# Kernel tuning notes

Measured on AMD Instinct MI355X. Metric: run time of the kernel, lower is better.

## Reference

```python
import jax, jax.numpy as jnp
import numpy as np

B, T, C, H, N = 4, 1024, 2048, 32, 64
DFF, DW, DV, DA, DG = 8192, 64, 32, 64, 128
GN_EPS = 64e-5  # RWKV7 ln_x GroupNorm eps


def _ln(x, w, b, eps=1e-5):
    m = x.mean(-1, keepdims=True)
    v = ((x - m) ** 2).mean(-1, keepdims=True)
    return (x - m) / jnp.sqrt(v + eps) * w + b


def _block(x, v_first, att_shift, ffn_shift, wkv_state,
           ln1_w, ln1_b, ln2_w, ln2_b,
           x_r, x_w, x_k, x_v, x_a, x_g,
           Wr, Wk, Wv, Wo,
           w0, w1, w2, v0, v1, v2, a0, a1, a2, g1, g2,
           k_k, k_a, r_k, lnx_w, lnx_b,
           ffn_xk, Wk_ffn, Wv_ffn):
    # ----- TimeMix -----
    xn = _ln(x, ln1_w, ln1_b)
    xx = jnp.concatenate([att_shift[:, None, :], xn[:, :-1]], axis=1) - xn
    xr = xn + xx * x_r
    xw = xn + xx * x_w
    xk_ = xn + xx * x_k
    xv = xn + xx * x_v
    xa = xn + xx * x_a
    xg = xn + xx * x_g

    r = xr @ Wr
    w = -jax.nn.softplus(-(w0 + jnp.tanh(xw @ w1) @ w2)) - 0.5  # <= -0.5
    k = xk_ @ Wk
    v = xv @ Wv
    # layer_id != 0: interpolate toward v_first
    v = v + (v_first - v) * jax.nn.sigmoid(v0 + (xv @ v1) @ v2)
    a = jax.nn.sigmoid(a0 + (xa @ a1) @ a2)
    g = jax.nn.sigmoid(xg @ g1) @ g2

    kk = (k * k_k).reshape(B, T, H, N)
    kk = kk / jnp.maximum(jnp.linalg.norm(kk, axis=-1, keepdims=True), 1e-12)
    k = k * (1.0 + (a - 1.0) * k_a)

    rh = r.reshape(B, T, H, N)
    wh = jnp.exp(-jnp.exp(w.reshape(B, T, H, N)))  # decay in (0,1)
    kh = k.reshape(B, T, H, N)
    vh = v.reshape(B, T, H, N)
    ah = a.reshape(B, T, H, N)
    aa = -kk
    bb = kk * ah

    def step(S, inp):
        # S: [B,H,N(value),N(key)]
        r_t, w_t, k_t, v_t, a_t, b_t = inp
        sa = jnp.einsum('bhvk,bhk->bhv', S, a_t)
        S = S * w_t[:, :, None, :] + sa[..., None] * b_t[:, :, None, :] + v_t[..., None] * k_t[:, :, None, :]
        y = jnp.einsum('bhvk,bhk->bhv', S, r_t)
        return S, y

    tm = lambda z: jnp.swapaxes(z, 0, 1)  # [B,T,H,N] -> [T,B,H,N]
    S_new, ys = jax.lax.scan(step, wkv_state, (tm(rh), tm(wh), tm(kh), tm(vh), tm(aa), tm(bb)))
    x_wkv = jnp.swapaxes(ys, 0, 1).reshape(B, T, C)

    # GroupNorm over H groups of size N (RWKV7 ln_x)
    xh = x_wkv.reshape(B, T, H, N)
    mu = xh.mean(-1, keepdims=True)
    var = ((xh - mu) ** 2).mean(-1, keepdims=True)
    x_wkv = ((xh - mu) / jnp.sqrt(var + GN_EPS)).reshape(B, T, C) * lnx_w + lnx_b

    resid = ((rh * kh * r_k).sum(-1, keepdims=True) * vh).reshape(B, T, C)
    x_wkv = x_wkv + resid
    att_out = (x_wkv * g) @ Wo
    x1 = x + att_out

    # ----- ChannelMix -----
    xn2 = _ln(x1, ln2_w, ln2_b)
    xx2 = jnp.concatenate([ffn_shift[:, None, :], xn2[:, :-1]], axis=1) - xn2
    xkf = xn2 + xx2 * ffn_xk
    kf = jnp.square(jax.nn.relu(xkf @ Wk_ffn))
    x_out = x1 + kf @ Wv_ffn
    return x_out, S_new


def setup_inputs() -> dict:
    ks = jax.random.split(jax.random.key(0), 48)
    rn = lambda i, sh, s=1.0: jax.random.normal(ks[i], sh, dtype=jnp.float32) * s
    return {
        'x': rn(0, (B, T, C)), 'v_first': rn(1, (B, T, C)),
        'att_shift': rn(2, (B, C)), 'ffn_shift': rn(3, (B, C)),
        'wkv_state': jnp.zeros((B, H, N, N), jnp.float32),
        'ln1_w': jnp.ones((C,), jnp.float32), 'ln1_b': jnp.zeros((C,), jnp.float32),
        'ln2_w': jnp.ones((C,), jnp.float32), 'ln2_b': jnp.zeros((C,), jnp.float32),
        'x_r': rn(4, (C,), 0.3), 'x_w': rn(5, (C,), 0.3), 'x_k': rn(6, (C,), 0.3),
        'x_v': rn(7, (C,), 0.3), 'x_a': rn(8, (C,), 0.3), 'x_g': rn(9, (C,), 0.3),
        'Wr': rn(10, (C, C), 0.02), 'Wk': rn(11, (C, C), 0.02),
        'Wv': rn(12, (C, C), 0.02), 'Wo': rn(13, (C, C), 0.02),
        'w0': rn(14, (C,), 0.3), 'w1': rn(15, (C, DW), 0.02), 'w2': rn(16, (DW, C), 0.02),
        'v0': rn(17, (C,), 0.3), 'v1': rn(18, (C, DV), 0.02), 'v2': rn(19, (DV, C), 0.02),
        'a0': rn(20, (C,), 0.3), 'a1': rn(21, (C, DA), 0.02), 'a2': rn(22, (DA, C), 0.02),
        'g1': rn(23, (C, DG), 0.02), 'g2': rn(24, (DG, C), 0.02),
        'k_k': rn(25, (C,), 0.1) + 0.7, 'k_a': rn(26, (C,), 0.1) + 0.7, 'r_k': rn(27, (H, N), 0.1),
        'lnx_w': jnp.ones((C,), jnp.float32), 'lnx_b': jnp.zeros((C,), jnp.float32),
        'ffn_xk': rn(28, (C,), 0.3), 'Wk_ffn': rn(29, (C, DFF), 0.02), 'Wv_ffn': rn(30, (DFF, C), 0.02),
    }


def reference(x, v_first, att_shift, ffn_shift, wkv_state,
              ln1_w, ln1_b, ln2_w, ln2_b,
              x_r, x_w, x_k, x_v, x_a, x_g,
              Wr, Wk, Wv, Wo,
              w0, w1, w2, v0, v1, v2, a0, a1, a2, g1, g2,
              k_k, k_a, r_k, lnx_w, lnx_b,
              ffn_xk, Wk_ffn, Wv_ffn):
    return _block(x, v_first, att_shift, ffn_shift, wkv_state,
                  ln1_w, ln1_b, ln2_w, ln2_b,
                  x_r, x_w, x_k, x_v, x_a, x_g,
                  Wr, Wk, Wv, Wo,
                  w0, w1, w2, v0, v1, v2, a0, a1, a2, g1, g2,
                  k_k, k_a, r_k, lnx_w, lnx_b,
                  ffn_xk, Wk_ffn, Wv_ffn)
```

## Files before the change

kernel.cpp:

```cpp
#include <hip/hip_runtime.h>
#include <cstdint>


typedef __attribute__((ext_vector_type(4))) float f32x4;
typedef __attribute__((ext_vector_type(8))) __bf16 bf16x8;
typedef __attribute__((ext_vector_type(8))) unsigned short us8;

#define DEV __device__ __forceinline__

DEV unsigned short f2b(float f) {
  union { float f; unsigned u; } v; v.f = f;
  unsigned r = v.u + 0x7fffu + ((v.u >> 16) & 1u);
  return (unsigned short)(r >> 16);
}
DEV float b2f(unsigned short u) {
  union { unsigned u; float f; } v; v.u = (unsigned)u << 16;
  return v.f;
}

DEV void gload16(const void* g, void* l) {
  void* gg = const_cast<void*>(g);
  __builtin_amdgcn_global_load_lds(
      (__attribute__((address_space(1))) unsigned int*)gg,
      (__attribute__((address_space(3))) unsigned int*)l, 16, 0, 0);
}

DEV float red8(float v) {
  v += __shfl_xor(v, 1);
  v += __shfl_xor(v, 2);
  v += __shfl_xor(v, 4);
  return v;
}


__global__ void k_transpose(const float* __restrict__ src,
                            unsigned short* __restrict__ dst, int R, int Cc) {
  __shared__ float tile[32][33];
  const int c0 = blockIdx.x * 32, r0 = blockIdx.y * 32;
  const int tx = threadIdx.x, ty = threadIdx.y;
  for (int i = ty; i < 32; i += 8)
    tile[i][tx] = src[(size_t)(r0 + i) * Cc + c0 + tx];
  __syncthreads();
  for (int i = ty; i < 32; i += 8)
    dst[(size_t)(c0 + i) * R + r0 + tx] = f2b(tile[tx][i]);
}

__global__ void k_wcat(const float* __restrict__ w1, const float* __restrict__ a1,
                       const float* __restrict__ v1, const float* __restrict__ g1,
                       const float* __restrict__ xw, const float* __restrict__ xa,
                       const float* __restrict__ xv, const float* __restrict__ xg,
                       unsigned short* __restrict__ dst) {
  const int i = blockIdx.x * 256 + threadIdx.x;
  if (i >= 384 * 4096) return;
  const int j = i >> 12, c = i & 4095;
  float val = 0.f;
  if (j < 288) {
    const float* W; const float* mix; int jj, D;
    if (j < 64)       { W = w1; mix = xw; jj = j;       D = 64;  }
    else if (j < 128) { W = a1; mix = xa; jj = j - 64;  D = 64;  }
    else if (j < 160) { W = v1; mix = xv; jj = j - 128; D = 32;  }
    else              { W = g1; mix = xg; jj = j - 160; D = 128; }
    const int cc = c & 2047;
    val = W[(size_t)cc * D + jj];
    if (c >= 2048) val *= mix[cc];
  }
  dst[i] = f2b(val);
}


DEV void breduce2(float& a, float& b, float* rbuf) {
#pragma unroll
  for (int m = 1; m < 64; m <<= 1) { a += __shfl_xor(a, m); b += __shfl_xor(b, m); }
  const int wid = threadIdx.x >> 6, lane = threadIdx.x & 63;
  if (lane == 0) { rbuf[wid] = a; rbuf[4 + wid] = b; }
  __syncthreads();
  a = rbuf[0] + rbuf[1] + rbuf[2] + rbuf[3];
  b = rbuf[4] + rbuf[5] + rbuf[6] + rbuf[7];
  __syncthreads();
}

__global__ __launch_bounds__(256)
void k_ln1_mix(const float* __restrict__ x, const float* __restrict__ shift,
               const float* __restrict__ lw, const float* __restrict__ lb,
               const float* __restrict__ mr, const float* __restrict__ mk,
               const float* __restrict__ mv,
               unsigned short* __restrict__ A2, unsigned short* __restrict__ xrb,
               unsigned short* __restrict__ xkb, unsigned short* __restrict__ xvb) {
  __shared__ float rbuf[8];
  const int m = blockIdx.x, tid = threadIdx.x;
  const int b = m >> 10, t = m & 1023;
  const float* xt = x + (size_t)m * 2048 + tid * 8;
  const float* xp = (t > 0) ? (x + (size_t)(m - 1) * 2048 + tid * 8)
                            : (shift + (size_t)b * 2048 + tid * 8);
  float vt[8], vp[8];
  *(float4*)&vt[0] = *(const float4*)(xt);
  *(float4*)&vt[4] = *(const float4*)(xt + 4);
  *(float4*)&vp[0] = *(const float4*)(xp);
  *(float4*)&vp[4] = *(const float4*)(xp + 4);
  float st = 0.f, sp = 0.f;
#pragma unroll
  for (int i = 0; i < 8; ++i) { st += vt[i]; sp += vp[i]; }
  breduce2(st, sp, rbuf);
  const float mt_ = st * (1.f / 2048.f), mp_ = sp * (1.f / 2048.f);
  float qt = 0.f, qp = 0.f;
#pragma unroll
  for (int i = 0; i < 8; ++i) {
    float d0 = vt[i] - mt_; qt += d0 * d0;
    float d1 = vp[i] - mp_; qp += d1 * d1;
  }
  breduce2(qt, qp, rbuf);
  const float rt = rsqrtf(qt * (1.f / 2048.f) + 1e-5f);
  const float rp = rsqrtf(qp * (1.f / 2048.f) + 1e-5f);
  const bool lnp = (t > 0);
#pragma unroll
  for (int i = 0; i < 8; ++i) {
    const int c = tid * 8 + i;
    const float wv = lw[c], bv = lb[c];
    const float xn = (vt[i] - mt_) * rt * wv + bv;
    const float pn = lnp ? ((vp[i] - mp_) * rp * wv + bv) : vp[i];
    const float xx = pn - xn;
    A2[(size_t)m * 4096 + c] = f2b(xn);
    A2[(size_t)m * 4096 + 2048 + c] = f2b(xx);
    xrb[(size_t)m * 2048 + c] = f2b(xn + xx * mr[c]);
    xkb[(size_t)m * 2048 + c] = f2b(xn + xx * mk[c]);
    xvb[(size_t)m * 2048 + c] = f2b(xn + xx * mv[c]);
  }
}

__global__ __launch_bounds__(256)
void k_ln2_mix(const float* __restrict__ x1, const float* __restrict__ shift,
               const float* __restrict__ lw, const float* __restrict__ lb,
               const float* __restrict__ mk, unsigned short* __restrict__ xkf) {
  __shared__ float rbuf[8];
  const int m = blockIdx.x, tid = threadIdx.x;
  const int b = m >> 10, t = m & 1023;
  const float* xt = x1 + (size_t)m * 2048 + tid * 8;
  const float* xp = (t > 0) ? (x1 + (size_t)(m - 1) * 2048 + tid * 8)
                            : (shift + (size_t)b * 2048 + tid * 8);
  float vt[8], vp[8];
  *(float4*)&vt[0] = *(const float4*)(xt);
  *(float4*)&vt[4] = *(const float4*)(xt + 4);
  *(float4*)&vp[0] = *(const float4*)(xp);
  *(float4*)&vp[4] = *(const float4*)(xp + 4);
  float st = 0.f, sp = 0.f;
#pragma unroll
  for (int i = 0; i < 8; ++i) { st += vt[i]; sp += vp[i]; }
  breduce2(st, sp, rbuf);
  const float mt_ = st * (1.f / 2048.f), mp_ = sp * (1.f / 2048.f);
  float qt = 0.f, qp = 0.f;
#pragma unroll
  for (int i = 0; i < 8; ++i) {
    float d0 = vt[i] - mt_; qt += d0 * d0;
    float d1 = vp[i] - mp_; qp += d1 * d1;
  }
  breduce2(qt, qp, rbuf);
  const float rt = rsqrtf(qt * (1.f / 2048.f) + 1e-5f);
  const float rp = rsqrtf(qp * (1.f / 2048.f) + 1e-5f);
  const bool lnp = (t > 0);
#pragma unroll
  for (int i = 0; i < 8; ++i) {
    const int c = tid * 8 + i;
    const float wv = lw[c], bv = lb[c];
    const float xn = (vt[i] - mt_) * rt * wv + bv;
    const float pn = lnp ? ((vp[i] - mp_) * rp * wv + bv) : vp[i];
    xkf[(size_t)m * 2048 + c] = f2b(xn + (pn - xn) * mk[c]);
  }
}


constexpr int EP_F32 = 0, EP_B16 = 1, EP_W = 2, EP_AB16 = 3, EP_VGB16 = 4,
              EP_RELU2 = 5, EP_ADDF = 6, EP_HACT = 7;

template <int EP>
DEV void ep_store(float acc, long row, long c, long ldc, float* Co,
                  unsigned short* Cob, const float* bias, const float* e0f,
                  const unsigned short* e0b) {
  const long idx = row * ldc + c;
  if constexpr (EP == EP_F32) {
    Co[idx] = acc;
  } else if constexpr (EP == EP_B16) {
    Cob[idx] = f2b(acc);
  } else if constexpr (EP == EP_W) {
    const float wv = bias[c] + acc;
    const float sp = log1pf(expf(-wv));
    const float w = -sp - 0.5f;
    Co[idx] = expf(-expf(w));
  } else if constexpr (EP == EP_AB16) {
    Cob[idx] = f2b(1.f / (1.f + expf(-(bias[c] + acc))));
  } else if constexpr (EP == EP_VGB16) {
    const float s = 1.f / (1.f + expf(-(bias[c] + acc)));
    const float vv = b2f(e0b[idx]);
    Cob[idx] = f2b(vv + (e0f[idx] - vv) * s);
  } else if constexpr (EP == EP_RELU2) {
    const float r = fmaxf(acc, 0.f);
    Cob[idx] = f2b(r * r);
  } else if constexpr (EP == EP_ADDF) {
    Co[idx] = acc + e0f[idx];
  } else if constexpr (EP == EP_HACT) {
    float vv = acc;
    if (c < 64) vv = tanhf(vv);
    else if (c >= 160) vv = 1.f / (1.f + expf(-vv));
    Cob[idx] = f2b(vv);
  }
}


template <int EP>
__global__ __launch_bounds__(256)
void gemm_bt(const unsigned short* __restrict__ A, long lda,
             const unsigned short* __restrict__ Bt, long ldb, long N, long K,
             long ldc, float* __restrict__ Co, unsigned short* __restrict__ Cob,
             const float* __restrict__ bias, const float* __restrict__ e0f,
             const unsigned short* __restrict__ e0b) {
  __shared__ unsigned short As[4096];
  __shared__ unsigned short Bs[4096];
  const int tid = threadIdx.x;
  const int wid = tid >> 6, lane = tid & 63;
  const long row0 = (long)blockIdx.x * 128, col0 = (long)blockIdx.y * 128;
  const int wm = (wid >> 1) * 64, wn = (wid & 1) * 64;
  f32x4 acc[4][4] = {};
  const int sr = tid >> 2, sk = (tid & 3) * 8;
  const unsigned short* gA = A + (row0 + sr) * lda + sk;
  const unsigned short* gB = Bt + (col0 + sr) * ldb + sk;
  unsigned short* lA = As + wid * 512;
  unsigned short* lB = Bs + wid * 512;
  const int fr = lane & 15, fk = (lane >> 4) * 8;

  for (long kb = 0; kb < K; kb += 32) {
    gload16(gA + kb, lA);
    gload16(gA + kb + 64 * lda, lA + 2048);
    gload16(gB + kb, lB);
    gload16(gB + kb + 64 * ldb, lB + 2048);
    __syncthreads();
    bf16x8 af[4], bq[4];
#pragma unroll
    for (int mt = 0; mt < 4; ++mt)
      af[mt] = *(const bf16x8*)(As + (wm + mt * 16 + fr) * 32 + fk);
#pragma unroll
    for (int nt = 0; nt < 4; ++nt)
      bq[nt] = *(const bf16x8*)(Bs + (wn + nt * 16 + fr) * 32 + fk);
#pragma unroll
    for (int mt = 0; mt < 4; ++mt)
#pragma unroll
      for (int nt = 0; nt < 4; ++nt)
        acc[mt][nt] = __builtin_amdgcn_mfma_f32_16x16x32_bf16(
            af[mt], bq[nt], acc[mt][nt], 0, 0, 0);
    __syncthreads();
  }
  const int fq = lane >> 4;
#pragma unroll
  for (int mt = 0; mt < 4; ++mt) {
#pragma unroll
    for (int nt = 0; nt < 4; ++nt) {
      const long c = col0 + wn + nt * 16 + fr;
      if (c < N) {
        const long rb = row0 + wm + mt * 16 + fq * 4;
#pragma unroll
        for (int rg = 0; rg < 4; ++rg)
          ep_store<EP>(acc[mt][nt][rg], rb + rg, c, ldc, Co, Cob, bias, e0f, e0b);
      }
    }
  }
}


template <int EP>
__global__ __launch_bounds__(512)
void gemm2(const unsigned short* __restrict__ A, long lda,
           const unsigned short* __restrict__ Bt, long ldb, long K, long ldc,
           float* __restrict__ Co, unsigned short* __restrict__ Cob,
           const float* __restrict__ e0f) {
  __shared__ unsigned short As[2][4096];
  __shared__ unsigned short Bs[2][8192];
  const int tid = threadIdx.x;
  const int wid = tid >> 6, lane = tid & 63;
  const long row0 = (long)blockIdx.x * 128, col0 = (long)blockIdx.y * 256;
  const int wm = (wid >> 2) * 64, wn = (wid & 3) * 64;
  f32x4 acc[4][4] = {};
  const int srow = tid >> 2;
  const int scol = 8 * ((tid & 3) ^ (srow & 3));
  const unsigned short* gA = A + (row0 + srow) * lda + scol;
  const unsigned short* gB1 = Bt + (col0 + srow) * ldb + scol;
  const unsigned short* gB2 = gB1 + 128 * ldb;
  const int fr = lane & 15, fc = lane >> 4;

#define STAGE2(buf, kb)                                   \
  {                                                       \
    gload16(gA + (kb), &As[buf][0] + wid * 512);          \
    gload16(gB1 + (kb), &Bs[buf][0] + wid * 512);         \
    gload16(gB2 + (kb), &Bs[buf][0] + 4096 + wid * 512);  \
  }

  STAGE2(0, 0)
  const int NT = (int)(K >> 5);
  int cur = 0;
  for (int kt = 0; kt < NT; ++kt) {
    if (kt + 1 < NT) {
      STAGE2(cur ^ 1, (long)(kt + 1) * 32)
      asm volatile("s_waitcnt vmcnt(3)" ::: "memory");
    } else {
      asm volatile("s_waitcnt vmcnt(0)" ::: "memory");
    }
    __builtin_amdgcn_s_barrier();
    asm volatile("" ::: "memory");
    bf16x8 af[4], bq[4];
#pragma unroll
    for (int mt = 0; mt < 4; ++mt) {
      const int r = wm + mt * 16 + fr;
      af[mt] = *(const bf16x8*)(&As[cur][0] + r * 32 + ((fc ^ (r & 3)) * 8));
    }
#pragma unroll
    for (int nt = 0; nt < 4; ++nt) {
      const int r = wn + nt * 16 + fr;
      bq[nt] = *(const bf16x8*)(&Bs[cur][0] + r * 32 + ((fc ^ (r & 3)) * 8));
    }
    __builtin_amdgcn_s_setprio(1);
#pragma unroll
    for (int mt = 0; mt < 4; ++mt)
#pragma unroll
      for (int nt = 0; nt < 4; ++nt)
        acc[mt][nt] = __builtin_amdgcn_mfma_f32_16x16x32_bf16(
            af[mt], bq[nt], acc[mt][nt], 0, 0, 0);
    __builtin_amdgcn_s_setprio(0);
    asm volatile("" ::: "memory");
    __builtin_amdgcn_s_barrier();
    cur ^= 1;
  }
#undef STAGE2
  const int fq = lane >> 4;
#pragma unroll
  for (int mt = 0; mt < 4; ++mt) {
#pragma unroll
    for (int nt = 0; nt < 4; ++nt) {
      const long c = col0 + wn + nt * 16 + fr;
      const long rb = row0 + wm + mt * 16 + fq * 4;
#pragma unroll
      for (int rg = 0; rg < 4; ++rg)
        ep_store<EP>(acc[mt][nt][rg], rb + rg, c, ldc, Co, Cob, nullptr, e0f,
                     nullptr);
    }
  }
}

__global__ __launch_bounds__(256)
void k_post(unsigned short* __restrict__ kio, unsigned short* __restrict__ abio,
            unsigned short* __restrict__ aao, const float* __restrict__ kkw,
            const float* __restrict__ kaw) {
  const int m = blockIdx.x, tid = threadIdx.x;
  const size_t base = (size_t)m * 2048 + tid * 8;
  us8 k8 = *(const us8*)(kio + base);
  us8 a8 = *(const us8*)(abio + base);
  float kk8[8], ka8[8];
  *(float4*)&kk8[0] = *(const float4*)(kkw + tid * 8);
  *(float4*)&kk8[4] = *(const float4*)(kkw + tid * 8 + 4);
  *(float4*)&ka8[0] = *(const float4*)(kaw + tid * 8);
  *(float4*)&ka8[4] = *(const float4*)(kaw + tid * 8 + 4);
  float kx[8], kv[8], av[8];
  float ss = 0.f;
#pragma unroll
  for (int i = 0; i < 8; ++i) {
    kv[i] = b2f(k8[i]); av[i] = b2f(a8[i]);
    kx[i] = kv[i] * kk8[i]; ss += kx[i] * kx[i];
  }
  ss = red8(ss);
  const float inv = 1.f / fmaxf(sqrtf(ss), 1e-12f);
  us8 kh8, aa8, bb8;
#pragma unroll
  for (int i = 0; i < 8; ++i) {
    const float kkn = kx[i] * inv;
    kh8[i] = f2b(kv[i] * (1.f + (av[i] - 1.f) * ka8[i]));
    aa8[i] = f2b(-kkn);
    bb8[i] = f2b(kkn * av[i]);
  }
  *(us8*)(kio + base) = kh8;
  *(us8*)(aao + base) = aa8;
  *(us8*)(abio + base) = bb8;
}


DEV float red16(float x) {
  union { float f; int i; } a, r;
  a.f = x; r.i = __builtin_amdgcn_update_dpp(0, a.i, 0xB1, 0xf, 0xf, true);
  x += r.f;
  a.f = x; r.i = __builtin_amdgcn_update_dpp(0, a.i, 0x4E, 0xf, 0xf, true);
  x += r.f;
  a.f = x; r.i = __builtin_amdgcn_update_dpp(0, a.i, 0x124, 0xf, 0xf, true);
  x += r.f;
  a.f = x; r.i = __builtin_amdgcn_update_dpp(0, a.i, 0x128, 0xf, 0xf, true);
  x += r.f;
  return x;
}

DEV void cv4(const uint2 q, float* o) {
  union { unsigned u; float f; } t;
  t.u = q.x << 16;          o[0] = t.f;
  t.u = q.x & 0xffff0000u;  o[1] = t.f;
  t.u = q.y << 16;          o[2] = t.f;
  t.u = q.y & 0xffff0000u;  o[3] = t.f;
}

__global__ __launch_bounds__(64)
void k_scan(const unsigned short* __restrict__ rp,
            const unsigned short* __restrict__ kp,
            const unsigned short* __restrict__ vp,
            const float* __restrict__ wp,
            const unsigned short* __restrict__ ap,
            const unsigned short* __restrict__ bp,
            const float* __restrict__ s0, unsigned short* __restrict__ yout,
            float* __restrict__ snew) {
  __shared__ float4 slots[8][49];
  __shared__ unsigned short ylds[1024][4];
  const int lane = threadIdx.x;
  const int bh = blockIdx.x & 127;
  const int rq = blockIdx.x >> 7;
  const int b = bh >> 5, h = bh & 31;
  const int kg = lane & 15, rl = lane >> 4;
  const int v = rq * 4 + rl, ks = kg * 4;
  const size_t off_bh = (size_t)b * 1024 * 2048 + (size_t)h * 64;

  float S[4];
  *(float4*)&S[0] = *(const float4*)(s0 + (((size_t)bh * 64 + v) * 64 + ks));

  const char* gp = nullptr;
  size_t gstep = 0;
  if (lane < 49) {
    if (lane < 32) {
      const int arr = lane >> 3, sub = lane & 7;
      const unsigned short* base = arr == 0 ? rp : arr == 1 ? kp
                                 : arr == 2 ? ap : bp;
      gp = (const char*)(base + off_bh + sub * 8);
      gstep = 4096;
    } else if (lane < 48) {
      gp = (const char*)(wp + off_bh + (lane - 32) * 4);
      gstep = 8192;
    } else {
      gp = (const char*)(vp + off_bh + (rq & ~1) * 4);
      gstep = 4096;
    }
  }
#pragma unroll
  for (int s = 0; s < 8; ++s) {
    if (lane < 49) gload16(gp, &slots[s][0]);
    gp += gstep;
  }

  for (int t = 0; t < 1024; ++t) {
    asm volatile("s_waitcnt vmcnt(7)" ::: "memory");
    const int sl = t & 7;
    const char* sb = (const char*)&slots[sl][0];
    uint2 r2 = *(const uint2*)(sb + kg * 8);
    uint2 k2 = *(const uint2*)(sb + 128 + kg * 8);
    uint2 a2 = *(const uint2*)(sb + 256 + kg * 8);
    uint2 b2 = *(const uint2*)(sb + 384 + kg * 8);
    float4 wf = *(const float4*)(sb + 512 + kg * 16);
    const unsigned short vfu =
        *(const unsigned short*)(sb + 768 + ((rq & 1) * 4 + rl) * 2);
    asm volatile("s_waitcnt lgkmcnt(0)" ::: "memory");
    if (lane < 49) gload16(gp, &slots[sl][0]);
    if (t < 1015) gp += gstep;

    float rr[4], kk[4], av[4], bv[4];
    cv4(r2, rr); cv4(k2, kk); cv4(a2, av); cv4(b2, bv);
    const float vv = b2f(vfu);
    float sa = S[0] * av[0] + S[1] * av[1] + S[2] * av[2] + S[3] * av[3];
    sa = red16(sa);
    float y;
    S[0] = S[0] * wf.x + sa * bv[0] + vv * kk[0]; y  = S[0] * rr[0];
    S[1] = S[1] * wf.y + sa * bv[1] + vv * kk[1]; y += S[1] * rr[1];
    S[2] = S[2] * wf.z + sa * bv[2] + vv * kk[2]; y += S[2] * rr[2];
    S[3] = S[3] * wf.w + sa * bv[3] + vv * kk[3]; y += S[3] * rr[3];
    y = red16(y);
    if (kg == 0) ylds[t][rl] = f2b(y);
  }

  *(float4*)(snew + (((size_t)bh * 64 + v) * 64 + ks)) = *(const float4*)&S[0];
  asm volatile("s_waitcnt lgkmcnt(0)" ::: "memory");
#pragma unroll 4
  for (int it = 0; it < 16; ++it) {
    const int t = lane + it * 64;
    const uint2 val = *(const uint2*)&ylds[t][0];
    *(uint2*)(yout + off_bh + (size_t)t * 2048 + rq * 4) = val;
  }
}


__global__ __launch_bounds__(256)
void k_gn(const unsigned short* __restrict__ y, const unsigned short* __restrict__ r,
          const unsigned short* __restrict__ kh, const unsigned short* __restrict__ vf,
          const unsigned short* __restrict__ g, const float* __restrict__ rk,
          const float* __restrict__ lw, const float* __restrict__ lb,
          unsigned short* __restrict__ ywg) {
  const int m = blockIdx.x, tid = threadIdx.x;
  const size_t base = (size_t)m * 2048 + tid * 8;
  us8 y8 = *(const us8*)(y + base);
  us8 r8 = *(const us8*)(r + base);
  us8 k8 = *(const us8*)(kh + base);
  us8 v8 = *(const us8*)(vf + base);
  us8 g8 = *(const us8*)(g + base);
  float yv[8];
  float rkv[8];
  *(float4*)&rkv[0] = *(const float4*)(rk + tid * 8);
  *(float4*)&rkv[4] = *(const float4*)(rk + tid * 8 + 4);
  float sy = 0.f, sd = 0.f;
#pragma unroll
  for (int i = 0; i < 8; ++i) {
    yv[i] = b2f(y8[i]);
    sy += yv[i];
    sd += b2f(r8[i]) * b2f(k8[i]) * rkv[i];
  }
  sy = red8(sy);
  sd = red8(sd);
  const float mu = sy * (1.f / 64.f);
  float sq = 0.f;
#pragma unroll
  for (int i = 0; i < 8; ++i) { const float d = yv[i] - mu; sq += d * d; }
  sq = red8(sq);
  const float rstd = rsqrtf(sq * (1.f / 64.f) + 64e-5f);
  us8 o8;
#pragma unroll
  for (int i = 0; i < 8; ++i) {
    const int c = tid * 8 + i;
    const float gn = (yv[i] - mu) * rstd * lw[c] + lb[c];
    o8[i] = f2b((gn + sd * b2f(v8[i])) * b2f(g8[i]));
  }
  *(us8*)(ywg + base) = o8;
}


extern "C" void kernel_launch(void* const* d_in, const int* in_sizes, int n_in,
                              void* d_out, int out_size, void* d_ws,
                              size_t ws_size, hipStream_t stream) {
  (void)in_sizes; (void)n_in; (void)out_size; (void)ws_size;
  const float* x         = (const float*)d_in[0];
  const float* v_first   = (const float*)d_in[1];
  const float* att_shift = (const float*)d_in[2];
  const float* ffn_shift = (const float*)d_in[3];
  const float* wkv0      = (const float*)d_in[4];
  const float* ln1w = (const float*)d_in[5];
  const float* ln1b = (const float*)d_in[6];
  const float* ln2w = (const float*)d_in[7];
  const float* ln2b = (const float*)d_in[8];
  const float* x_r = (const float*)d_in[9];
  const float* x_w = (const float*)d_in[10];
  const float* x_k = (const float*)d_in[11];
  const float* x_v = (const float*)d_in[12];
  const float* x_a = (const float*)d_in[13];
  const float* x_g = (const float*)d_in[14];
  const float* Wr = (const float*)d_in[15];
  const float* Wk = (const float*)d_in[16];
  const float* Wv = (const float*)d_in[17];
  const float* Wo = (const float*)d_in[18];
  const float* w0 = (const float*)d_in[19];
  const float* w1 = (const float*)d_in[20];
  const float* w2 = (const float*)d_in[21];
  const float* v0 = (const float*)d_in[22];
  const float* v1 = (const float*)d_in[23];
  const float* v2 = (const float*)d_in[24];
  const float* a0 = (const float*)d_in[25];
  const float* a1 = (const float*)d_in[26];
  const float* a2 = (const float*)d_in[27];
  const float* g1 = (const float*)d_in[28];
  const float* g2 = (const float*)d_in[29];
  const float* k_k = (const float*)d_in[30];
  const float* k_a = (const float*)d_in[31];
  const float* r_k = (const float*)d_in[32];
  const float* lnxw = (const float*)d_in[33];
  const float* lnxb = (const float*)d_in[34];
  const float* ffn_xk = (const float*)d_in[35];
  const float* Wkf = (const float*)d_in[36];
  const float* Wvf = (const float*)d_in[37];

  char* ws = (char*)d_ws;
  constexpr size_t OFF_TWR   = 0;
  constexpr size_t OFF_TWK   = 8388608;
  constexpr size_t OFF_TWV   = 16777216;
  constexpr size_t OFF_TWO   = 25165824;
  constexpr size_t OFF_TW2   = 33554432;
  constexpr size_t OFF_TA2   = 33816576;
  constexpr size_t OFF_TV2   = 34078720;
  constexpr size_t OFF_TG2   = 34209792;
  constexpr size_t OFF_TWCAT = 34734080;
  constexpr size_t OFF_HACT  = 37879808;
  constexpr size_t OFF_GBUF  = 40239104;
  constexpr size_t OFF_WH    = 57016320;
  constexpr size_t OFF_R     = 90570752;
  constexpr size_t OFF_KH    = 107347968;
  constexpr size_t OFF_VF    = 124125184;
  constexpr size_t OFF_AA    = 140902400;
  constexpr size_t OFF_BB    = 157679616;

  unsigned short* tWr = (unsigned short*)(ws + OFF_TWR);
  unsigned short* tWk = (unsigned short*)(ws + OFF_TWK);
  unsigned short* tWv = (unsigned short*)(ws + OFF_TWV);
  unsigned short* tWo = (unsigned short*)(ws + OFF_TWO);
  unsigned short* tw2 = (unsigned short*)(ws + OFF_TW2);
  unsigned short* ta2 = (unsigned short*)(ws + OFF_TA2);
  unsigned short* tv2 = (unsigned short*)(ws + OFF_TV2);
  unsigned short* tg2 = (unsigned short*)(ws + OFF_TG2);
  unsigned short* tWcat = (unsigned short*)(ws + OFF_TWCAT);
  unsigned short* Hact  = (unsigned short*)(ws + OFF_HACT);
  unsigned short* gbuf  = (unsigned short*)(ws + OFF_GBUF);
  unsigned short* tWvfh = (unsigned short*)(ws + OFF_GBUF);
  unsigned short* act2  = (unsigned short*)(ws + OFF_WH);
  float*          whb   = (float*)(ws + OFF_WH);
  unsigned short* ywg   = (unsigned short*)(ws + OFF_WH);
  unsigned short* kf    = (unsigned short*)(ws + OFF_WH);
  unsigned short* bxr   = (unsigned short*)(ws + OFF_AA);
  unsigned short* bxk   = (unsigned short*)(ws + OFF_BB);
  unsigned short* bxv   = (unsigned short*)(ws + OFF_VF);
  unsigned short* rbuf  = (unsigned short*)(ws + OFF_R);
  unsigned short* khb   = (unsigned short*)(ws + OFF_KH);
  unsigned short* vfb   = (unsigned short*)(ws + OFF_VF);
  unsigned short* aab   = (unsigned short*)(ws + OFF_AA);
  unsigned short* bbb   = (unsigned short*)(ws + OFF_BB);
  unsigned short* vraw  = (unsigned short*)(ws + OFF_AA);
  unsigned short* abuf  = (unsigned short*)(ws + OFF_BB);
  float*          x1    = (float*)(ws + OFF_R);
  unsigned short* xkf   = (unsigned short*)(ws + OFF_VF);
  unsigned short* tWkf  = (unsigned short*)(ws + OFF_AA);
  float* out = (float*)d_out;
  float* snew = out + 8388608;

  const dim3 tb(32, 8);
  k_transpose<<<dim3(64, 64), tb, 0, stream>>>(Wr, tWr, 2048, 2048);
  k_transpose<<<dim3(64, 64), tb, 0, stream>>>(Wk, tWk, 2048, 2048);
  k_transpose<<<dim3(64, 64), tb, 0, stream>>>(Wv, tWv, 2048, 2048);
  k_transpose<<<dim3(64, 64), tb, 0, stream>>>(Wo, tWo, 2048, 2048);
  k_transpose<<<dim3(64, 2), tb, 0, stream>>>(w2, tw2, 64, 2048);
  k_transpose<<<dim3(64, 2), tb, 0, stream>>>(a2, ta2, 64, 2048);
  k_transpose<<<dim3(64, 1), tb, 0, stream>>>(v2, tv2, 32, 2048);
  k_transpose<<<dim3(64, 4), tb, 0, stream>>>(g2, tg2, 128, 2048);
  k_wcat<<<6144, 256, 0, stream>>>(w1, a1, v1, g1, x_w, x_a, x_v, x_g, tWcat);

  k_ln1_mix<<<4096, 256, 0, stream>>>(x, att_shift, ln1w, ln1b, x_r, x_k, x_v,
                                      act2, bxr, bxk, bxv);
  gemm2<EP_B16><<<dim3(32, 8), 512, 0, stream>>>(
      bxr, 2048, tWr, 2048, 2048, 2048, nullptr, rbuf, nullptr);
  gemm2<EP_B16><<<dim3(32, 8), 512, 0, stream>>>(
      bxk, 2048, tWk, 2048, 2048, 2048, nullptr, khb, nullptr);
  gemm2<EP_B16><<<dim3(32, 8), 512, 0, stream>>>(
      bxv, 2048, tWv, 2048, 2048, 2048, nullptr, vraw, nullptr);
  gemm_bt<EP_HACT><<<dim3(32, 3), 256, 0, stream>>>(
      act2, 4096, tWcat, 4096, 288, 4096, 288, nullptr, Hact, nullptr, nullptr, nullptr);
  gemm_bt<EP_W><<<dim3(32, 16), 256, 0, stream>>>(
      Hact + 0, 288, tw2, 64, 2048, 64, 2048, whb, nullptr, w0, nullptr, nullptr);
  gemm_bt<EP_AB16><<<dim3(32, 16), 256, 0, stream>>>(
      Hact + 64, 288, ta2, 64, 2048, 64, 2048, nullptr, abuf, a0, nullptr, nullptr);
  gemm_bt<EP_VGB16><<<dim3(32, 16), 256, 0, stream>>>(
      Hact + 128, 288, tv2, 32, 2048, 32, 2048, nullptr, vfb, v0, v_first, vraw);
  gemm_bt<EP_B16><<<dim3(32, 16), 256, 0, stream>>>(
      Hact + 160, 288, tg2, 128, 2048, 128, 2048, nullptr, gbuf, nullptr, nullptr, nullptr);
  k_post<<<4096, 256, 0, stream>>>(khb, abuf, aab, k_k, k_a);

  k_scan<<<2048, 64, 0, stream>>>(rbuf, khb, vfb, whb, aab, bbb, wkv0,
                                  (unsigned short*)out, snew);
  k_gn<<<4096, 256, 0, stream>>>((const unsigned short*)out, rbuf, khb, vfb,
                                 gbuf, r_k, lnxw, lnxb, ywg);

  gemm2<EP_ADDF><<<dim3(32, 8), 512, 0, stream>>>(
      ywg, 2048, tWo, 2048, 2048, 2048, x1, nullptr, x);

  k_ln2_mix<<<4096, 256, 0, stream>>>(x1, ffn_shift, ln2w, ln2b, ffn_xk, xkf);
  k_transpose<<<dim3(256, 64), tb, 0, stream>>>(Wkf, tWkf, 2048, 8192);
  gemm2<EP_RELU2><<<dim3(32, 16), 512, 0, stream>>>(
      xkf, 2048, tWkf, 2048, 2048, 4096, nullptr, kf, nullptr);
  k_transpose<<<dim3(64, 128), tb, 0, stream>>>(Wvf, tWvfh, 4096, 2048);
  gemm2<EP_ADDF><<<dim3(32, 8), 512, 0, stream>>>(
      kf, 4096, tWvfh, 4096, 4096, 2048, out, nullptr, x1);
  gemm2<EP_RELU2><<<dim3(32, 16), 512, 0, stream>>>(
      xkf, 2048, tWkf + (size_t)4096 * 2048, 2048, 2048, 4096, nullptr, kf, nullptr);
  k_transpose<<<dim3(64, 128), tb, 0, stream>>>(Wvf + (size_t)4096 * 2048, tWvfh,
                                                4096, 2048);
  gemm2<EP_ADDF><<<dim3(32, 8), 512, 0, stream>>>(
      kf, 4096, tWvfh, 4096, 4096, 2048, out, nullptr, out);
}
```

Before: 1.277 ms.

## Split WKV scan across twice as many blocks with two state columns per lane

New measurement: 1.413 ms. +10.6%, slower.

```diff
diff --git a/kernel.cpp b/kernel.cpp
--- a/kernel.cpp
+++ b/kernel.cpp
@@ -391,12 +391,10 @@
   return x;
 }
 
-DEV void cv4(const uint2 q, float* o) {
+DEV void cv2(const unsigned q, float* o) {
   union { unsigned u; float f; } t;
-  t.u = q.x << 16;          o[0] = t.f;
-  t.u = q.x & 0xffff0000u;  o[1] = t.f;
-  t.u = q.y << 16;          o[2] = t.f;
-  t.u = q.y & 0xffff0000u;  o[3] = t.f;
+  t.u = q << 16;          o[0] = t.f;
+  t.u = q & 0xffff0000u;  o[1] = t.f;
 }
 
 __global__ __launch_bounds__(64)
@@ -408,18 +406,18 @@
             const unsigned short* __restrict__ bp,
             const float* __restrict__ s0, unsigned short* __restrict__ yout,
             float* __restrict__ snew) {
-  __shared__ float4 slots[8][49];
-  __shared__ unsigned short ylds[1024][4];
+  __shared__ float4 slots[6][49];
+  __shared__ unsigned short ylds[1024][2];
   const int lane = threadIdx.x;
   const int bh = blockIdx.x & 127;
   const int rq = blockIdx.x >> 7;
   const int b = bh >> 5, h = bh & 31;
-  const int kg = lane & 15, rl = lane >> 4;
-  const int v = rq * 4 + rl, ks = kg * 4;
+  const int kg = lane & 31, rl = lane >> 5;
+  const int v = rq * 2 + rl, ks = kg * 2;
   const size_t off_bh = (size_t)b * 1024 * 2048 + (size_t)h * 64;
 
-  float S[4];
-  *(float4*)&S[0] = *(const float4*)(s0 + (((size_t)bh * 64 + v) * 64 + ks));
+  float S[2];
+  *(float2*)&S[0] = *(const float2*)(s0 + (((size_t)bh * 64 + v) * 64 + ks));
 
   const char* gp = nullptr;
   size_t gstep = 0;
@@ -434,52 +432,52 @@
       gp = (const char*)(wp + off_bh + (lane - 32) * 4);
       gstep = 8192;
     } else {
-      gp = (const char*)(vp + off_bh + (rq & ~1) * 4);
+      gp = (const char*)(vp + off_bh + (rq & ~3) * 2);
       gstep = 4096;
     }
   }
 #pragma unroll
-  for (int s = 0; s < 8; ++s) {
+  for (int s = 0; s < 6; ++s) {
     if (lane < 49) gload16(gp, &slots[s][0]);
     gp += gstep;
   }
 
   for (int t = 0; t < 1024; ++t) {
-    asm volatile("s_waitcnt vmcnt(7)" ::: "memory");
-    const int sl = t & 7;
+    asm volatile("s_waitcnt vmcnt(5)" ::: "memory");
+    const int sl = t % 6;
     const char* sb = (const char*)&slots[sl][0];
-    uint2 r2 = *(const uint2*)(sb + kg * 8);
-    uint2 k2 = *(const uint2*)(sb + 128 + kg * 8);
-    uint2 a2 = *(const uint2*)(sb + 256 + kg * 8);
-    uint2 b2 = *(const uint2*)(sb + 384 + kg * 8);
-    float4 wf = *(const float4*)(sb + 512 + kg * 16);
+    unsigned r1 = *(const unsigned*)(sb + kg * 4);
+    unsigned k1 = *(const unsigned*)(sb + 128 + kg * 4);
+    unsigned a1 = *(const unsigned*)(sb + 256 + kg * 4);
+    unsigned b1 = *(const unsigned*)(sb + 384 + kg * 4);
+    float2 wf = *(const float2*)(sb + 512 + kg * 8);
     const unsigned short vfu =
-        *(const unsigned short*)(sb + 768 + ((rq & 1) * 4 + rl) * 2);
+        *(const unsigned short*)(sb + 768 + ((rq & 3) * 2 + rl) * 2);
     asm volatile("s_waitcnt lgkmcnt(0)" ::: "memory");
     if (lane < 49) gload16(gp, &slots[sl][0]);
-    if (t < 1015) gp += gstep;
-
-    float rr[4], kk[4], av[4], bv[4];
-    cv4(r2, rr); cv4(k2, kk); cv4(a2, av); cv4(b2, bv);
+    if (t < 1017) gp += gstep;
+
+    float rr[2], kk[2], av[2], bv[2];
+    cv2(r1, rr); cv2(k1, kk); cv2(a1, av); cv2(b1, bv);
     const float vv = b2f(vfu);
-    float sa = S[0] * av[0] + S[1] * av[1] + S[2] * av[2] + S[3] * av[3];
+    float sa = S[0] * av[0] + S[1] * av[1];
     sa = red16(sa);
+    sa += __shfl_xor(sa, 16);
     float y;
     S[0] = S[0] * wf.x + sa * bv[0] + vv * kk[0]; y  = S[0] * rr[0];
     S[1] = S[1] * wf.y + sa * bv[1] + vv * kk[1]; y += S[1] * rr[1];
-    S[2] = S[2] * wf.z + sa * bv[2] + vv * kk[2]; y += S[2] * rr[2];
-    S[3] = S[3] * wf.w + sa * bv[3] + vv * kk[3]; y += S[3] * rr[3];
     y = red16(y);
+    y += __shfl_xor(y, 16);
     if (kg == 0) ylds[t][rl] = f2b(y);
   }
 
-  *(float4*)(snew + (((size_t)bh * 64 + v) * 64 + ks)) = *(const float4*)&S[0];
+  *(float2*)(snew + (((size_t)bh * 64 + v) * 64 + ks)) = *(const float2*)&S[0];
   asm volatile("s_waitcnt lgkmcnt(0)" ::: "memory");
 #pragma unroll 4
   for (int it = 0; it < 16; ++it) {
     const int t = lane + it * 64;
-    const uint2 val = *(const uint2*)&ylds[t][0];
-    *(uint2*)(yout + off_bh + (size_t)t * 2048 + rq * 4) = val;
+    const unsigned val = *(const unsigned*)&ylds[t][0];
+    *(unsigned*)(yout + off_bh + (size_t)t * 2048 + rq * 2) = val;
   }
 }
 
@@ -652,7 +650,7 @@
       Hact + 160, 288, tg2, 128, 2048, 128, 2048, nullptr, gbuf, nullptr, nullptr, nullptr);
   k_post<<<4096, 256, 0, stream>>>(khb, abuf, aab, k_k, k_a);
 
-  k_scan<<<2048, 64, 0, stream>>>(rbuf, khb, vfb, whb, aab, bbb, wkv0,
+  k_scan<<<4096, 64, 0, stream>>>(rbuf, khb, vfb, whb, aab, bbb, wkv0,
                                   (unsigned short*)out, snew);
   k_gn<<<4096, 256, 0, stream>>>((const unsigned short*)out, rbuf, khb, vfb,
                                  gbuf, r_k, lnxw, lnxb, ywg);
```

## Fuse four low-rank up-projection GEMMs into one block-diagonal GEMM

Applied to the files above, without the earlier changes.

Measured after the change: 1.299 ms. About the same (+1.7%).

```diff
diff --git a/kernel.cpp b/kernel.cpp
--- a/kernel.cpp
+++ b/kernel.cpp
@@ -64,6 +64,21 @@
     val = W[(size_t)cc * D + jj];
     if (c >= 2048) val *= mix[cc];
   }
+  dst[i] = f2b(val);
+}
+
+__global__ void k_wup(const float* __restrict__ w2, const float* __restrict__ a2,
+                      const float* __restrict__ v2, const float* __restrict__ g2,
+                      unsigned short* __restrict__ dst) {
+  const int i = blockIdx.x * 256 + threadIdx.x;
+  if (i >= 8192 * 288) return;
+  const int n = i / 288, k = i - n * 288;
+  const int p = n >> 11, j = n & 2047;
+  float val = 0.f;
+  if (p == 0)      { if (k < 64)              val = w2[(size_t)k * 2048 + j]; }
+  else if (p == 1) { if (k >= 64 && k < 128)  val = a2[(size_t)(k - 64) * 2048 + j]; }
+  else if (p == 2) { if (k >= 128 && k < 160) val = v2[(size_t)(k - 128) * 2048 + j]; }
+  else             { if (k >= 160)            val = g2[(size_t)(k - 160) * 2048 + j]; }
   dst[i] = f2b(val);
 }
 
@@ -168,29 +183,18 @@
 }
 
 
-constexpr int EP_F32 = 0, EP_B16 = 1, EP_W = 2, EP_AB16 = 3, EP_VGB16 = 4,
-              EP_RELU2 = 5, EP_ADDF = 6, EP_HACT = 7;
+constexpr int EP_F32 = 0, EP_B16 = 1, EP_RELU2 = 5, EP_ADDF = 6, EP_HACT = 7;
 
 template <int EP>
 DEV void ep_store(float acc, long row, long c, long ldc, float* Co,
                   unsigned short* Cob, const float* bias, const float* e0f,
                   const unsigned short* e0b) {
   const long idx = row * ldc + c;
+  (void)bias; (void)e0b;
   if constexpr (EP == EP_F32) {
     Co[idx] = acc;
   } else if constexpr (EP == EP_B16) {
     Cob[idx] = f2b(acc);
-  } else if constexpr (EP == EP_W) {
-    const float wv = bias[c] + acc;
-    const float sp = log1pf(expf(-wv));
-    const float w = -sp - 0.5f;
-    Co[idx] = expf(-expf(w));
-  } else if constexpr (EP == EP_AB16) {
-    Cob[idx] = f2b(1.f / (1.f + expf(-(bias[c] + acc))));
-  } else if constexpr (EP == EP_VGB16) {
-    const float s = 1.f / (1.f + expf(-(bias[c] + acc)));
-    const float vv = b2f(e0b[idx]);
-    Cob[idx] = f2b(vv + (e0f[idx] - vv) * s);
   } else if constexpr (EP == EP_RELU2) {
     const float r = fmaxf(acc, 0.f);
     Cob[idx] = f2b(r * r);
@@ -338,6 +342,103 @@
       for (int rg = 0; rg < 4; ++rg)
         ep_store<EP>(acc[mt][nt][rg], rb + rg, c, ldc, Co, Cob, nullptr, e0f,
                      nullptr);
+    }
+  }
+}
+
+
+__global__ __launch_bounds__(512)
+void gemm_up4(const unsigned short* __restrict__ A,
+              const unsigned short* __restrict__ Bt,
+              float* __restrict__ whb, unsigned short* __restrict__ abuf,
+              unsigned short* __restrict__ vfb, unsigned short* __restrict__ gbuf,
+              const float* __restrict__ w0, const float* __restrict__ a0,
+              const float* __restrict__ v0,
+              const unsigned short* __restrict__ vraw,
+              const float* __restrict__ vfirst) {
+  __shared__ unsigned short As[2][4096];
+  __shared__ unsigned short Bs[2][8192];
+  const int tid = threadIdx.x;
+  const int wid = tid >> 6, lane = tid & 63;
+  const long row0 = (long)blockIdx.x * 128, col0 = (long)blockIdx.y * 256;
+  const int wm = (wid >> 2) * 64, wn = (wid & 3) * 64;
+  f32x4 acc[4][4] = {};
+  const int srow = tid >> 2;
+  const int scol = 8 * ((tid & 3) ^ (srow & 3));
+  const unsigned short* gA = A + (row0 + srow) * 288 + scol;
+  const unsigned short* gB1 = Bt + (col0 + srow) * 288 + scol;
+  const unsigned short* gB2 = gB1 + 128 * 288;
+  const int fr = lane & 15, fc = lane >> 4;
+
+#define STAGEU(buf, kb)                                   \
+  {                                                       \
+    gload16(gA + (kb), &As[buf][0] + wid * 512);          \
+    gload16(gB1 + (kb), &Bs[buf][0] + wid * 512);         \
+    gload16(gB2 + (kb), &Bs[buf][0] + 4096 + wid * 512);  \
+  }
+
+  STAGEU(0, 0)
+  int cur = 0;
+  for (int kt = 0; kt < 9; ++kt) {
+    if (kt + 1 < 9) {
+      STAGEU(cur ^ 1, (long)(kt + 1) * 32)
+      asm volatile("s_waitcnt vmcnt(3)" ::: "memory");
+    } else {
+      asm volatile("s_waitcnt vmcnt(0)" ::: "memory");
+    }
+    __builtin_amdgcn_s_barrier();
+    asm volatile("" ::: "memory");
+    bf16x8 af[4], bq[4];
+#pragma unroll
+    for (int mt = 0; mt < 4; ++mt) {
+      const int r = wm + mt * 16 + fr;
+      af[mt] = *(const bf16x8*)(&As[cur][0] + r * 32 + ((fc ^ (r & 3)) * 8));
+    }
+#pragma unroll
+    for (int nt = 0; nt < 4; ++nt) {
+      const int r = wn + nt * 16 + fr;
+      bq[nt] = *(const bf16x8*)(&Bs[cur][0] + r * 32 + ((fc ^ (r & 3)) * 8));
+    }
+    __builtin_amdgcn_s_setprio(1);
+#pragma unroll
+    for (int mt = 0; mt < 4; ++mt)
+#pragma unroll
+      for (int nt = 0; nt < 4; ++nt)
+        acc[mt][nt] = __builtin_amdgcn_mfma_f32_16x16x32_bf16(
+            af[mt], bq[nt], acc[mt][nt], 0, 0, 0);
+    __builtin_amdgcn_s_setprio(0);
+    asm volatile("" ::: "memory");
+    __builtin_amdgcn_s_barrier();
+    cur ^= 1;
+  }
+#undef STAGEU
+  const int fq = lane >> 4;
+  const int p = (int)(blockIdx.y >> 3);
+#pragma unroll
+  for (int mt = 0; mt < 4; ++mt) {
+#pragma unroll
+    for (int nt = 0; nt < 4; ++nt) {
+      const long c = col0 + wn + nt * 16 + fr;
+      const long cc = c & 2047;
+      const long rb = row0 + wm + mt * 16 + fq * 4;
+#pragma unroll
+      for (int rg = 0; rg < 4; ++rg) {
+        const float av = acc[mt][nt][rg];
+        const long idx = (rb + rg) * 2048 + cc;
+        if (p == 0) {
+          const float wv = w0[cc] + av;
+          const float sp = log1pf(expf(-wv));
+          whb[idx] = expf(-expf(-sp - 0.5f));
+        } else if (p == 1) {
+          abuf[idx] = f2b(1.f / (1.f + expf(-(a0[cc] + av))));
+        } else if (p == 2) {
+          const float s = 1.f / (1.f + expf(-(v0[cc] + av)));
+          const float vv = b2f(vraw[idx]);
+          vfb[idx] = f2b(vv + (vfirst[idx] - vv) * s);
+        } else {
+          gbuf[idx] = f2b(av);
+        }
+      }
     }
   }
 }
@@ -575,10 +676,6 @@
   constexpr size_t OFF_TWK   = 8388608;
   constexpr size_t OFF_TWV   = 16777216;
   constexpr size_t OFF_TWO   = 25165824;
-  constexpr size_t OFF_TW2   = 33554432;
-  constexpr size_t OFF_TA2   = 33816576;
-  constexpr size_t OFF_TV2   = 34078720;
-  constexpr size_t OFF_TG2   = 34209792;
   constexpr size_t OFF_TWCAT = 34734080;
   constexpr size_t OFF_HACT  = 37879808;
   constexpr size_t OFF_GBUF  = 40239104;
@@ -588,15 +685,12 @@
   constexpr size_t OFF_VF    = 124125184;
   constexpr size_t OFF_AA    = 140902400;
   constexpr size_t OFF_BB    = 157679616;
+  constexpr size_t OFF_TWUP  = 174456832;
 
   unsigned short* tWr = (unsigned short*)(ws + OFF_TWR);
   unsigned short* tWk = (unsigned short*)(ws + OFF_TWK);
   unsigned short* tWv = (unsigned short*)(ws + OFF_TWV);
   unsigned short* tWo = (unsigned short*)(ws + OFF_TWO);
-  unsigned short* tw2 = (unsigned short*)(ws + OFF_TW2);
-  unsigned short* ta2 = (unsigned short*)(ws + OFF_TA2);
-  unsigned short* tv2 = (unsigned short*)(ws + OFF_TV2);
-  unsigned short* tg2 = (unsigned short*)(ws + OFF_TG2);
   unsigned short* tWcat = (unsigned short*)(ws + OFF_TWCAT);
   unsigned short* Hact  = (unsigned short*)(ws + OFF_HACT);
   unsigned short* gbuf  = (unsigned short*)(ws + OFF_GBUF);
@@ -618,6 +712,7 @@
   float*          x1    = (float*)(ws + OFF_R);
   unsigned short* xkf   = (unsigned short*)(ws + OFF_VF);
   unsigned short* tWkf  = (unsigned short*)(ws + OFF_AA);
+  unsigned short* tWup  = (unsigned short*)(ws + OFF_TWUP);
   float* out = (float*)d_out;
   float* snew = out + 8388608;
 
@@ -626,11 +721,8 @@
   k_transpose<<<dim3(64, 64), tb, 0, stream>>>(Wk, tWk, 2048, 2048);
   k_transpose<<<dim3(64, 64), tb, 0, stream>>>(Wv, tWv, 2048, 2048);
   k_transpose<<<dim3(64, 64), tb, 0, stream>>>(Wo, tWo, 2048, 2048);
-  k_transpose<<<dim3(64, 2), tb, 0, stream>>>(w2, tw2, 64, 2048);
-  k_transpose<<<dim3(64, 2), tb, 0, stream>>>(a2, ta2, 64, 2048);
-  k_transpose<<<dim3(64, 1), tb, 0, stream>>>(v2, tv2, 32, 2048);
-  k_transpose<<<dim3(64, 4), tb, 0, stream>>>(g2, tg2, 128, 2048);
   k_wcat<<<6144, 256, 0, stream>>>(w1, a1, v1, g1, x_w, x_a, x_v, x_g, tWcat);
+  k_wup<<<9216, 256, 0, stream>>>(w2, a2, v2, g2, tWup);
 
   k_ln1_mix<<<4096, 256, 0, stream>>>(x, att_shift, ln1w, ln1b, x_r, x_k, x_v,
                                       act2, bxr, bxk, bxv);
@@ -642,14 +734,8 @@
       bxv, 2048, tWv, 2048, 2048, 2048, nullptr, vraw, nullptr);
   gemm_bt<EP_HACT><<<dim3(32, 3), 256, 0, stream>>>(
       act2, 4096, tWcat, 4096, 288, 4096, 288, nullptr, Hact, nullptr, nullptr, nullptr);
-  gemm_bt<EP_W><<<dim3(32, 16), 256, 0, stream>>>(
-      Hact + 0, 288, tw2, 64, 2048, 64, 2048, whb, nullptr, w0, nullptr, nullptr);
-  gemm_bt<EP_AB16><<<dim3(32, 16), 256, 0, stream>>>(
-      Hact + 64, 288, ta2, 64, 2048, 64, 2048, nullptr, abuf, a0, nullptr, nullptr);
-  gemm_bt<EP_VGB16><<<dim3(32, 16), 256, 0, stream>>>(
-      Hact + 128, 288, tv2, 32, 2048, 32, 2048, nullptr, vfb, v0, v_first, vraw);
-  gemm_bt<EP_B16><<<dim3(32, 16), 256, 0, stream>>>(
-      Hact + 160, 288, tg2, 128, 2048, 128, 2048, nullptr, gbuf, nullptr, nullptr, nullptr);
+  gemm_up4<<<dim3(32, 32), 512, 0, stream>>>(
+      Hact, tWup, whb, abuf, vfb, gbuf, w0, a0, v0, vraw, v_first);
   k_post<<<4096, 256, 0, stream>>>(khb, abuf, aab, k_k, k_a);
 
   k_scan<<<2048, 64, 0, stream>>>(rbuf, khb, vfb, whb, aab, bbb, wkv0,
```
